# Kernel tuning notes

Hardware: AMD Instinct MI355X
Metric: run time of the kernel (lower is better)

## Reference

```python
import jax, jax.numpy as jnp
import numpy as np


def _squash_global(v):
    # Faithful to torch: v.norm() with no dim -> global Frobenius norm (scalar).
    n2 = jnp.sum(v * v)
    n = jnp.sqrt(n2)
    scale = n2 / (1.0 + n2)
    return scale * v / n


def setup_inputs() -> dict:
    key = jax.random.key(0)
    k1, k2 = jax.random.split(key)
    B, R, Ci = 128, 1152, 8
    C, O = 10, 16
    x = jax.random.normal(k1, (B, R, Ci), dtype=jnp.float32)
    W = jax.random.normal(k2, (C, R, Ci, O), dtype=jnp.float32)  # routing_weights ~ randn
    return {"x": x, "W": W, "num_iterations": 3}


def reference(x, W, num_iterations):
    # prediction_vectors: [C, B, R, 1, O]
    u = jnp.einsum('bri,crio->cbro', x, W)[:, :, :, None, :]
    logits = jnp.zeros_like(u)
    v = None
    for _ in range(num_iterations):
        # batch_softmax: cat over dim0 + legacy softmax(dim=1 of 4D) == softmax over
        # the num_route_nodes axis (axis 2 here).
        c = jax.nn.softmax(logits, axis=2)
        s = jnp.sum(c * u, axis=2, keepdims=True)  # [C, B, 1, 1, O]
        v = _squash_global(s)
        logits = logits + u * v
    return v
```

## Files before the change

### kernel.cpp

```cpp
#include <hip/hip_runtime.h>
#include <math.h>

#define Bn   128
#define Rn   1152
#define CIn  8
#define Cn   10
#define On   16
#define BO   2048
#define CBO  20480
#define RC   12
#define GRID 480
#define NTHR 512
#define LOG2E 1.4426950408889634f
#define INV_R 8.6805555e-4f


__global__ __launch_bounds__(256)
void transpose_x(const float* __restrict__ X, float* __restrict__ XT,
                 float* __restrict__ TL)
{
    const int r = blockIdx.x;
    const int b = threadIdx.x & 127;
    const int g = threadIdx.x >> 7;
    float4 v = *(const float4*)(X + (size_t)b * (Rn * CIn) + r * CIn + g * 4);
    ((float4*)XT)[r * 256 + g * 128 + b] = v;
    const int zi = blockIdx.x * 256 + threadIdx.x;
    if (zi < 25604) ((float4*)TL)[zi] = make_float4(0.f, 0.f, 0.f, 0.f);
}

template<int PASS>
__global__ __launch_bounds__(NTHR, 4)
void pass_kernel(const float* __restrict__ XT, const float* __restrict__ W,
                 float* __restrict__ TL, float* __restrict__ out)
{
    __shared__ __align__(16) float smem[8 * 64 * 18];
    __shared__ float sred[16];
    __shared__ int sdone;
    float (*wlds)[128]   = (float (*)[128])smem;
    float (*red)[64][18] = (float (*)[64][18])smem;

    float* T1 = TL;
    float* T2 = TL + CBO;
    float* L2 = TL + 2 * CBO;
    float* T3 = TL + 3 * CBO;
    float* L3 = TL + 4 * CBO;
    unsigned* ticket = (unsigned*)(TL + 5 * CBO);

    const int blk  = blockIdx.x;
    const int c    = blk / 48;
    const int rem  = blk - c * 48;
    const int bh   = rem / 24;
    const int segq = rem - bh * 24;
    const int tid  = threadIdx.x;
    const int w    = tid >> 6;
    const int lane = tid & 63;
    const int b    = bh * 64 + lane;
    const int oh   = w >> 2;
    const int sw   = w & 3;
    const int ohs  = __builtin_amdgcn_readfirstlane(oh * 8);

    {
        const float4* gw4 = (const float4*)(W + (size_t)(c * Rn + segq * 48) * 128);
        float4* sw4 = (float4*)smem;
        #pragma unroll
        for (int k = 0; k < 3; ++k)
            sw4[tid + k * 512] = gw4[tid + k * 512];
    }

    float vs[8];
    if (PASS > 1) {
        float n2a = 0.f, n2b = 0.f;
        const float4* T1v = (const float4*)T1;
        if (PASS == 2) {
            for (int i = tid; i < 5120; i += NTHR) {
                float4 v = T1v[i];
                v.x *= INV_R; v.y *= INV_R; v.z *= INV_R; v.w *= INV_R;
                n2a += v.x * v.x + v.y * v.y + v.z * v.z + v.w * v.w;
            }
        } else {
            const float4* T2v = (const float4*)T2;
            const float4* L2v = (const float4*)L2;
            for (int i = tid; i < 5120; i += NTHR) {
                float4 v = T1v[i];
                v.x *= INV_R; v.y *= INV_R; v.z *= INV_R; v.w *= INV_R;
                n2a += v.x * v.x + v.y * v.y + v.z * v.z + v.w * v.w;
                float4 t = T2v[i], l = L2v[i];
                float s0 = t.x / l.x, s1 = t.y / l.y, s2 = t.z / l.z, s3 = t.w / l.w;
                n2b += s0 * s0 + s1 * s1 + s2 * s2 + s3 * s3;
            }
        }
        #pragma unroll
        for (int d = 1; d < 64; d <<= 1) {
            n2a += __shfl_xor(n2a, d);
            n2b += __shfl_xor(n2b, d);
        }
        if (lane == 0) { sred[w] = n2a; sred[8 + w] = n2b; }
        __syncthreads();
        n2a = sred[0] + sred[1] + sred[2] + sred[3] +
              sred[4] + sred[5] + sred[6] + sred[7];
        n2b = sred[8] + sred[9] + sred[10] + sred[11] +
              sred[12] + sred[13] + sred[14] + sred[15];

        const float c1 = n2a / ((1.f + n2a) * sqrtf(n2a)) * (LOG2E * INV_R);
        const float* s1p = T1 + c * BO + b * On + ohs;
        if (PASS == 2) {
            #pragma unroll
            for (int q = 0; q < 2; ++q) {
                float4 v = *(const float4*)(s1p + q * 4);
                vs[q*4+0] = c1 * v.x; vs[q*4+1] = c1 * v.y;
                vs[q*4+2] = c1 * v.z; vs[q*4+3] = c1 * v.w;
            }
        } else {
            const float c2 = n2b / ((1.f + n2b) * sqrtf(n2b)) * LOG2E;
            const float* t2p = T2 + c * BO + b * On + ohs;
            const float* l2p = L2 + c * BO + b * On + ohs;
            #pragma unroll
            for (int q = 0; q < 2; ++q) {
                float4 v = *(const float4*)(s1p + q * 4);
                float4 t = *(const float4*)(t2p + q * 4);
                float4 l = *(const float4*)(l2p + q * 4);
                vs[q*4+0] = c1 * v.x + c2 * (t.x / l.x);
                vs[q*4+1] = c1 * v.y + c2 * (t.y / l.y);
                vs[q*4+2] = c1 * v.z + c2 * (t.z / l.z);
                vs[q*4+3] = c1 * v.w + c2 * (t.w / l.w);
            }
        }
    }

    float tacc[8], lacc[8];
    #pragma unroll
    for (int o = 0; o < 8; ++o) { tacc[o] = 0.0f; lacc[o] = 0.0f; }

    __syncthreads();

    const float4* XT4 = (const float4*)XT;
    for (int rr = 0; rr < RC; ++rr) {
        const int lrow = sw * RC + rr;
        const int r    = segq * 48 + lrow;
        const float4 xa = XT4[r * 256 + b];
        const float4 xb = XT4[r * 256 + 128 + b];
        const float xi[8] = { xa.x, xa.y, xa.z, xa.w, xb.x, xb.y, xb.z, xb.w };

        float u[8];
        #pragma unroll
        for (int o = 0; o < 8; ++o) u[o] = 0.0f;
        #pragma unroll
        for (int i = 0; i < 8; ++i) {
            const float4 w0 = *(const float4*)&wlds[lrow][i * 16 + ohs + 0];
            const float4 w1 = *(const float4*)&wlds[lrow][i * 16 + ohs + 4];
            const float x = xi[i];
            u[0] = fmaf(x, w0.x, u[0]);  u[1] = fmaf(x, w0.y, u[1]);
            u[2] = fmaf(x, w0.z, u[2]);  u[3] = fmaf(x, w0.w, u[3]);
            u[4] = fmaf(x, w1.x, u[4]);  u[5] = fmaf(x, w1.y, u[5]);
            u[6] = fmaf(x, w1.z, u[6]);  u[7] = fmaf(x, w1.w, u[7]);
        }
        #pragma unroll
        for (int o = 0; o < 8; ++o) {
            if (PASS == 1) {
                tacc[o] += u[o];
            } else {
                const float e = exp2f(u[o] * vs[o]);
                lacc[o] += e;
                tacc[o] = fmaf(e, u[o], tacc[o]);
            }
        }
    }

    __syncthreads();

    #pragma unroll
    for (int o = 0; o < 8; ++o) {
        red[w][lane][o] = tacc[o];
        if (PASS > 1) red[w][lane][8 + o] = lacc[o];
    }
    __syncthreads();

    {
        const int oh2  = tid >> 8;
        const int rem2 = tid & 255;
        const int bl   = rem2 >> 2;
        const int oq   = rem2 & 3;
        const int bg   = bh * 64 + bl;
        float* Tslot = (PASS == 1) ? T1 : (PASS == 2) ? T2 : T3;
        float* Lslot = (PASS == 2) ? L2 : L3;
        const int idx = c * BO + bg * On + oh2 * 8 + oq * 2;
        #pragma unroll
        for (int q = 0; q < 2; ++q) {
            const int o = oq * 2 + q;
            atomicAdd(Tslot + idx + q,
                      red[oh2*4+0][bl][o] + red[oh2*4+1][bl][o] +
                      red[oh2*4+2][bl][o] + red[oh2*4+3][bl][o]);
            if (PASS > 1)
                atomicAdd(Lslot + idx + q,
                          red[oh2*4+0][bl][8+o] + red[oh2*4+1][bl][8+o] +
                          red[oh2*4+2][bl][8+o] + red[oh2*4+3][bl][8+o]);
        }
    }

    if (PASS == 3) {
        __syncthreads();
        if (tid == 0) {
            __threadfence();
            sdone = (atomicAdd(ticket, 1u) == GRID - 1);
        }
        __syncthreads();
        if (sdone) {
            __threadfence();
            const float4* T3v = (const float4*)T3;
            const float4* L3v = (const float4*)L3;
            float acc = 0.f;
            for (int i = tid; i < 5120; i += NTHR) {
                float4 t = T3v[i], l = L3v[i];
                float s0 = t.x / l.x, s1 = t.y / l.y, s2 = t.z / l.z, s3 = t.w / l.w;
                acc += s0 * s0 + s1 * s1 + s2 * s2 + s3 * s3;
            }
            #pragma unroll
            for (int d = 1; d < 64; d <<= 1) acc += __shfl_xor(acc, d);
            if (lane == 0) sred[w] = acc;
            __syncthreads();
            float n2 = 0.f;
            #pragma unroll
            for (int k = 0; k < 8; ++k) n2 += sred[k];
            const float c3 = n2 / ((1.f + n2) * sqrtf(n2));
            for (int i = tid; i < 5120; i += NTHR) {
                float4 t = T3v[i], l = L3v[i];
                float4 o4;
                o4.x = c3 * t.x / l.x; o4.y = c3 * t.y / l.y;
                o4.z = c3 * t.z / l.z; o4.w = c3 * t.w / l.w;
                ((float4*)out)[i] = o4;
            }
        }
    }
}

extern "C" void kernel_launch(void* const* d_in, const int* in_sizes, int n_in,
                              void* d_out, int out_size, void* d_ws, size_t ws_size,
                              hipStream_t stream)
{
    const float* X = (const float*)d_in[0];
    const float* W = (const float*)d_in[1];
    float* ws = (float*)d_ws;
    float* XT = ws;
    float* TL = XT + Rn * Bn * CIn;
    float* out = (float*)d_out;

    transpose_x<<<Rn, 256, 0, stream>>>(X, XT, TL);
    pass_kernel<1><<<GRID, NTHR, 0, stream>>>(XT, W, TL, out);
    pass_kernel<2><<<GRID, NTHR, 0, stream>>>(XT, W, TL, out);
    pass_kernel<3><<<GRID, NTHR, 0, stream>>>(XT, W, TL, out);
}
```

Baseline: 152.1 us.

## Materialize prediction vectors in pass 1 and stream them in routing passes

Pass 1 now writes the full prediction tensor u (C*B*R*O floats) to workspace while also reducing it. Passes 2 and 3 become lightweight streaming kernels that read u instead of recomputing the x·W einsum and reloading W into LDS. Each routing row is reduced by one wavefront, with plain stores replacing atomics. This trades recompute for roughly 94 MB of extra global writes plus two full reads, and relies on the workspace being large enough for u.

```diff
diff --git a/kernel.cpp b/kernel.cpp
--- a/kernel.cpp
+++ b/kernel.cpp
@@ -9,8 +9,11 @@
 #define BO   2048
 #define CBO  20480
 #define RC   12
-#define GRID 480
-#define NTHR 512
+#define GRID1 480
+#define NT1  512
+#define NBLK2 320
+#define NT2  256
+#define UROW 18432
 #define LOG2E 1.4426950408889634f
 #define INV_R 8.6805555e-4f
 
@@ -28,23 +31,14 @@
     if (zi < 25604) ((float4*)TL)[zi] = make_float4(0.f, 0.f, 0.f, 0.f);
 }
 
-template<int PASS>
-__global__ __launch_bounds__(NTHR, 4)
-void pass_kernel(const float* __restrict__ XT, const float* __restrict__ W,
-                 float* __restrict__ TL, float* __restrict__ out)
+__global__ __launch_bounds__(NT1, 4)
+void pass1_kernel(const float* __restrict__ XT, const float* __restrict__ W,
+                  float* __restrict__ TL, float* __restrict__ U)
 {
     __shared__ __align__(16) float smem[8 * 64 * 18];
-    __shared__ float sred[16];
-    __shared__ int sdone;
     float (*wlds)[128]   = (float (*)[128])smem;
     float (*red)[64][18] = (float (*)[64][18])smem;
-
     float* T1 = TL;
-    float* T2 = TL + CBO;
-    float* L2 = TL + 2 * CBO;
-    float* T3 = TL + 3 * CBO;
-    float* L3 = TL + 4 * CBO;
-    unsigned* ticket = (unsigned*)(TL + 5 * CBO);
 
     const int blk  = blockIdx.x;
     const int c    = blk / 48;
@@ -67,78 +61,23 @@
             sw4[tid + k * 512] = gw4[tid + k * 512];
     }
 
-    float vs[8];
-    if (PASS > 1) {
-        float n2a = 0.f, n2b = 0.f;
-        const float4* T1v = (const float4*)T1;
-        if (PASS == 2) {
-            for (int i = tid; i < 5120; i += NTHR) {
-                float4 v = T1v[i];
-                v.x *= INV_R; v.y *= INV_R; v.z *= INV_R; v.w *= INV_R;
-                n2a += v.x * v.x + v.y * v.y + v.z * v.z + v.w * v.w;
-            }
-        } else {
-            const float4* T2v = (const float4*)T2;
-            const float4* L2v = (const float4*)L2;
-            for (int i = tid; i < 5120; i += NTHR) {
-                float4 v = T1v[i];
-                v.x *= INV_R; v.y *= INV_R; v.z *= INV_R; v.w *= INV_R;
-                n2a += v.x * v.x + v.y * v.y + v.z * v.z + v.w * v.w;
-                float4 t = T2v[i], l = L2v[i];
-                float s0 = t.x / l.x, s1 = t.y / l.y, s2 = t.z / l.z, s3 = t.w / l.w;
-                n2b += s0 * s0 + s1 * s1 + s2 * s2 + s3 * s3;
-            }
-        }
-        #pragma unroll
-        for (int d = 1; d < 64; d <<= 1) {
-            n2a += __shfl_xor(n2a, d);
-            n2b += __shfl_xor(n2b, d);
-        }
-        if (lane == 0) { sred[w] = n2a; sred[8 + w] = n2b; }
-        __syncthreads();
-        n2a = sred[0] + sred[1] + sred[2] + sred[3] +
-              sred[4] + sred[5] + sred[6] + sred[7];
-        n2b = sred[8] + sred[9] + sred[10] + sred[11] +
-              sred[12] + sred[13] + sred[14] + sred[15];
-
-        const float c1 = n2a / ((1.f + n2a) * sqrtf(n2a)) * (LOG2E * INV_R);
-        const float* s1p = T1 + c * BO + b * On + ohs;
-        if (PASS == 2) {
-            #pragma unroll
-            for (int q = 0; q < 2; ++q) {
-                float4 v = *(const float4*)(s1p + q * 4);
-                vs[q*4+0] = c1 * v.x; vs[q*4+1] = c1 * v.y;
-                vs[q*4+2] = c1 * v.z; vs[q*4+3] = c1 * v.w;
-            }
-        } else {
-            const float c2 = n2b / ((1.f + n2b) * sqrtf(n2b)) * LOG2E;
-            const float* t2p = T2 + c * BO + b * On + ohs;
-            const float* l2p = L2 + c * BO + b * On + ohs;
-            #pragma unroll
-            for (int q = 0; q < 2; ++q) {
-                float4 v = *(const float4*)(s1p + q * 4);
-                float4 t = *(const float4*)(t2p + q * 4);
-                float4 l = *(const float4*)(l2p + q * 4);
-                vs[q*4+0] = c1 * v.x + c2 * (t.x / l.x);
-                vs[q*4+1] = c1 * v.y + c2 * (t.y / l.y);
-                vs[q*4+2] = c1 * v.z + c2 * (t.z / l.z);
-                vs[q*4+3] = c1 * v.w + c2 * (t.w / l.w);
-            }
-        }
-    }
-
-    float tacc[8], lacc[8];
+    float tacc[8];
     #pragma unroll
-    for (int o = 0; o < 8; ++o) { tacc[o] = 0.0f; lacc[o] = 0.0f; }
+    for (int o = 0; o < 8; ++o) tacc[o] = 0.0f;
 
     __syncthreads();
 
     const float4* XT4 = (const float4*)XT;
+    const float4* xp  = XT4 + (size_t)(segq * 48 + sw * RC) * 256 + b;
+    float* ubase = U + ((size_t)(c * Bn + b) * Rn + (segq * 48 + sw * RC)) * On + ohs;
+
+    float4 xa = xp[0];
+    float4 xb = xp[128];
     for (int rr = 0; rr < RC; ++rr) {
+        const int nx = (rr + 1 < RC) ? (rr + 1) : rr;
+        const float4 nxa = xp[nx * 256];
+        const float4 nxb = xp[nx * 256 + 128];
         const int lrow = sw * RC + rr;
-        const int r    = segq * 48 + lrow;
-        const float4 xa = XT4[r * 256 + b];
-        const float4 xb = XT4[r * 256 + 128 + b];
         const float xi[8] = { xa.x, xa.y, xa.z, xa.w, xb.x, xb.y, xb.z, xb.w };
 
         float u[8];
@@ -154,25 +93,17 @@
             u[4] = fmaf(x, w1.x, u[4]);  u[5] = fmaf(x, w1.y, u[5]);
             u[6] = fmaf(x, w1.z, u[6]);  u[7] = fmaf(x, w1.w, u[7]);
         }
-        #pragma unroll
-        for (int o = 0; o < 8; ++o) {
-            if (PASS == 1) {
-                tacc[o] += u[o];
-            } else {
-                const float e = exp2f(u[o] * vs[o]);
-                lacc[o] += e;
-                tacc[o] = fmaf(e, u[o], tacc[o]);
-            }
-        }
+        *(float4*)(ubase + (size_t)rr * On)     = make_float4(u[0], u[1], u[2], u[3]);
+        *(float4*)(ubase + (size_t)rr * On + 4) = make_float4(u[4], u[5], u[6], u[7]);
+        #pragma unroll
+        for (int o = 0; o < 8; ++o) tacc[o] += u[o];
+        xa = nxa; xb = nxb;
     }
 
     __syncthreads();
 
     #pragma unroll
-    for (int o = 0; o < 8; ++o) {
-        red[w][lane][o] = tacc[o];
-        if (PASS > 1) red[w][lane][8 + o] = lacc[o];
-    }
+    for (int o = 0; o < 8; ++o) red[w][lane][o] = tacc[o];
     __syncthreads();
 
     {
@@ -181,27 +112,118 @@
         const int bl   = rem2 >> 2;
         const int oq   = rem2 & 3;
         const int bg   = bh * 64 + bl;
-        float* Tslot = (PASS == 1) ? T1 : (PASS == 2) ? T2 : T3;
-        float* Lslot = (PASS == 2) ? L2 : L3;
         const int idx = c * BO + bg * On + oh2 * 8 + oq * 2;
         #pragma unroll
         for (int q = 0; q < 2; ++q) {
             const int o = oq * 2 + q;
-            atomicAdd(Tslot + idx + q,
+            atomicAdd(T1 + idx + q,
                       red[oh2*4+0][bl][o] + red[oh2*4+1][bl][o] +
                       red[oh2*4+2][bl][o] + red[oh2*4+3][bl][o]);
-            if (PASS > 1)
-                atomicAdd(Lslot + idx + q,
-                          red[oh2*4+0][bl][8+o] + red[oh2*4+1][bl][8+o] +
-                          red[oh2*4+2][bl][8+o] + red[oh2*4+3][bl][8+o]);
-        }
+        }
+    }
+}
+
+template<int PASS>
+__global__ __launch_bounds__(NT2)
+void stream_pass(const float* __restrict__ U, float* __restrict__ TL,
+                 float* __restrict__ out)
+{
+    __shared__ float sA[4], sB[4];
+    __shared__ int sdone;
+    float* T1 = TL;
+    float* T2 = TL + CBO;
+    float* L2 = TL + 2 * CBO;
+    float* T3 = TL + 3 * CBO;
+    float* L3 = TL + 4 * CBO;
+    unsigned* ticket = (unsigned*)(TL + 5 * CBO);
+
+    const int tid  = threadIdx.x;
+    const int blk  = blockIdx.x;
+    const int w    = tid >> 6;
+    const int lane = tid & 63;
+    const int og   = lane & 3;
+
+    float n2a = 0.f, n2b = 0.f;
+    {
+        const float4* T1v = (const float4*)T1;
+        if (PASS == 2) {
+            for (int i = tid; i < 5120; i += NT2) {
+                float4 v = T1v[i];
+                float s0 = v.x*INV_R, s1 = v.y*INV_R, s2 = v.z*INV_R, s3 = v.w*INV_R;
+                n2a += s0*s0 + s1*s1 + s2*s2 + s3*s3;
+            }
+        } else {
+            const float4* T2v = (const float4*)T2;
+            const float4* L2v = (const float4*)L2;
+            for (int i = tid; i < 5120; i += NT2) {
+                float4 v = T1v[i];
+                float s0 = v.x*INV_R, s1 = v.y*INV_R, s2 = v.z*INV_R, s3 = v.w*INV_R;
+                n2a += s0*s0 + s1*s1 + s2*s2 + s3*s3;
+                float4 t = T2v[i], l = L2v[i];
+                float q0 = t.x/l.x, q1 = t.y/l.y, q2 = t.z/l.z, q3 = t.w/l.w;
+                n2b += q0*q0 + q1*q1 + q2*q2 + q3*q3;
+            }
+        }
+        #pragma unroll
+        for (int d = 1; d < 64; d <<= 1) {
+            n2a += __shfl_xor(n2a, d);
+            n2b += __shfl_xor(n2b, d);
+        }
+        if (lane == 0) { sA[w] = n2a; sB[w] = n2b; }
+        __syncthreads();
+        n2a = sA[0] + sA[1] + sA[2] + sA[3];
+        n2b = sB[0] + sB[1] + sB[2] + sB[3];
+    }
+
+    const int row = blk * 4 + w;
+    const float c1 = n2a / ((1.f + n2a) * sqrtf(n2a)) * (LOG2E * INV_R);
+
+    float4 vsv;
+    {
+        float4 t1 = *(const float4*)(T1 + row * On + og * 4);
+        vsv.x = c1 * t1.x; vsv.y = c1 * t1.y; vsv.z = c1 * t1.z; vsv.w = c1 * t1.w;
+        if (PASS == 3) {
+            const float c2 = n2b / ((1.f + n2b) * sqrtf(n2b)) * LOG2E;
+            float4 t2 = *(const float4*)(T2 + row * On + og * 4);
+            float4 l2 = *(const float4*)(L2 + row * On + og * 4);
+            vsv.x += c2 * (t2.x / l2.x); vsv.y += c2 * (t2.y / l2.y);
+            vsv.z += c2 * (t2.z / l2.z); vsv.w += c2 * (t2.w / l2.w);
+        }
+    }
+
+    const float4* Uv = (const float4*)(U + (size_t)row * UROW);
+    float4 Ta = make_float4(0.f,0.f,0.f,0.f), La = make_float4(0.f,0.f,0.f,0.f);
+    #pragma unroll 8
+    for (int k = 0; k < 72; ++k) {
+        const float4 uv = Uv[k * 64 + lane];
+        const float e0 = exp2f(uv.x * vsv.x);
+        const float e1 = exp2f(uv.y * vsv.y);
+        const float e2 = exp2f(uv.z * vsv.z);
+        const float e3 = exp2f(uv.w * vsv.w);
+        Ta.x = fmaf(e0, uv.x, Ta.x); La.x += e0;
+        Ta.y = fmaf(e1, uv.y, Ta.y); La.y += e1;
+        Ta.z = fmaf(e2, uv.z, Ta.z); La.z += e2;
+        Ta.w = fmaf(e3, uv.w, Ta.w); La.w += e3;
+    }
+    #pragma unroll
+    for (int d = 4; d < 64; d <<= 1) {
+        Ta.x += __shfl_xor(Ta.x, d); Ta.y += __shfl_xor(Ta.y, d);
+        Ta.z += __shfl_xor(Ta.z, d); Ta.w += __shfl_xor(Ta.w, d);
+        La.x += __shfl_xor(La.x, d); La.y += __shfl_xor(La.y, d);
+        La.z += __shfl_xor(La.z, d); La.w += __shfl_xor(La.w, d);
+    }
+    float* Ts = (PASS == 2) ? T2 : T3;
+    float* Ls = (PASS == 2) ? L2 : L3;
+    if (lane < 4) {
+        *(float4*)(Ts + row * On + lane * 4) = Ta;
+        *(float4*)(Ls + row * On + lane * 4) = La;
     }
 
     if (PASS == 3) {
         __syncthreads();
         if (tid == 0) {
             __threadfence();
-            sdone = (atomicAdd(ticket, 1u) == GRID - 1);
+            sdone = (atomicAdd(ticket, 1u) == NBLK2 - 1);
         }
         __syncthreads();
         if (sdone) {
@@ -209,20 +231,18 @@
             const float4* T3v = (const float4*)T3;
             const float4* L3v = (const float4*)L3;
             float acc = 0.f;
-            for (int i = tid; i < 5120; i += NTHR) {
+            for (int i = tid; i < 5120; i += NT2) {
                 float4 t = T3v[i], l = L3v[i];
-                float s0 = t.x / l.x, s1 = t.y / l.y, s2 = t.z / l.z, s3 = t.w / l.w;
-                acc += s0 * s0 + s1 * s1 + s2 * s2 + s3 * s3;
+                float s0 = t.x/l.x, s1 = t.y/l.y, s2 = t.z/l.z, s3 = t.w/l.w;
+                acc += s0*s0 + s1*s1 + s2*s2 + s3*s3;
             }
             #pragma unroll
             for (int d = 1; d < 64; d <<= 1) acc += __shfl_xor(acc, d);
-            if (lane == 0) sred[w] = acc;
+            if (lane == 0) sA[w] = acc;
             __syncthreads();
-            float n2 = 0.f;
-            #pragma unroll
-            for (int k = 0; k < 8; ++k) n2 += sred[k];
+            const float n2 = sA[0] + sA[1] + sA[2] + sA[3];
             const float c3 = n2 / ((1.f + n2) * sqrtf(n2));
-            for (int i = tid; i < 5120; i += NTHR) {
+            for (int i = tid; i < 5120; i += NT2) {
                 float4 t = T3v[i], l = L3v[i];
                 float4 o4;
                 o4.x = c3 * t.x / l.x; o4.y = c3 * t.y / l.y;
@@ -242,10 +262,11 @@
     float* ws = (float*)d_ws;
     float* XT = ws;
     float* TL = XT + Rn * Bn * CIn;
+    float* U  = TL + 102416;
     float* out = (float*)d_out;
 
     transpose_x<<<Rn, 256, 0, stream>>>(X, XT, TL);
-    pass_kernel<1><<<GRID, NTHR, 0, stream>>>(XT, W, TL, out);
-    pass_kernel<2><<<GRID, NTHR, 0, stream>>>(XT, W, TL, out);
-    pass_kernel<3><<<GRID, NTHR, 0, stream>>>(XT, W, TL, out);
-}
+    pass1_kernel<<<GRID1, NT1, 0, stream>>>(XT, W, TL, U);
+    stream_pass<2><<<NBLK2, NT2, 0, stream>>>(U, TL, out);
+    stream_pass<3><<<NBLK2, NT2, 0, stream>>>(U, TL, out);
+}
```

Result: slower. 190.1 us (+25.0%).
